# Optimization experiments

Hardware: AMD Instinct MI355X
Metric: run time of the kernel (lower is better)

Reference implementation:

```python
import jax, jax.numpy as jnp
import numpy as np

B, C, H, W = 4, 256, 64, 64
NUM_HEADS, HIDDEN = 2, 64


def setup_inputs() -> dict:
    key = jax.random.key(0)
    k1, k2, k3 = jax.random.split(key, 3)
    x = jax.random.normal(k1, (B, C, H, W), dtype=jnp.float32)
    # per-head fused QKV 1x1 conv weights: [num_heads, 3*hidden, C]
    embed_w = jax.random.normal(k2, (NUM_HEADS, 3 * HIDDEN, C), dtype=jnp.float32) * (2.0 / C) ** 0.5
    embed_b = jnp.zeros((NUM_HEADS, 3 * HIDDEN), dtype=jnp.float32)
    # output ConvTranspose2d kernel-1 weight: [in=hidden*heads, out=C]
    out_w = jax.random.normal(k3, (HIDDEN * NUM_HEADS, C), dtype=jnp.float32) * (2.0 / C) ** 0.5
    out_b = jnp.zeros((C,), dtype=jnp.float32)
    return {"x": x, "embed_w": embed_w, "embed_b": embed_b, "out_w": out_w, "out_b": out_b}


def reference(x, embed_w, embed_b, out_w, out_b):
    b, c, h, w = x.shape
    n = h * w
    scale = c ** (-0.5)  # scaled=True uses in_channels**-0.5
    xf = x.reshape(b, c, n)  # [B,C,N]
    # fused QKV projection for all heads (1x1 conv == channel matmul)
    qkv = jnp.einsum('bcn,hdc->bhdn', xf, embed_w) + embed_b[None, :, :, None]  # [B,Hh,3*hc,N]
    q, k, v = jnp.split(qkv, 3, axis=2)  # each [B,Hh,hc,N]
    # attention over flattened spatial positions
    attn = jax.nn.softmax(jnp.einsum('bhcm,bhcn->bhmn', q, k) * scale, axis=-1)  # [B,Hh,N,N]
    o = jnp.einsum('bhmn,bhcn->bhcm', attn, v)  # [B,Hh,hc,N]
    o = o.reshape(b, -1, n)  # concat heads -> [B, hc*Hh, N]
    # output 1x1 transpose conv: sum over input channel dim d of weight[d, c]
    out = jnp.einsum('bdn,dc->bcn', o, out_w) + out_b[None, :, None]
    out = out.reshape(b, c, h, w)
    return out + x  # residual=True
```

## Files before the change

kernel.cpp:

```cpp
#include <hip/hip_runtime.h>

#define B_SZ  4
#define C_IN  256
#define N_POS 4096
#define NH    2
#define HC    64

typedef __attribute__((ext_vector_type(8))) __bf16 bf16x8;
typedef __attribute__((ext_vector_type(4))) float  f32x4;
typedef unsigned short u16;

__device__ __forceinline__ u16 f2bf(float f) {
  unsigned u = __float_as_uint(f);
  u = u + 0x7FFF + ((u >> 16) & 1);
  return (u16)(u >> 16);
}

#if __has_builtin(__builtin_amdgcn_exp2f)
  #define EXP2(x) __builtin_amdgcn_exp2f(x)
#else
  #define EXP2(x) exp2f(x)
#endif

__device__ __forceinline__ unsigned cvtpk_bf16(float lo, float hi) {
  unsigned r;
  asm("v_cvt_pk_bf16_f32 %0, %1, %2" : "=v"(r) : "v"(lo), "v"(hi));
  return r;
}

__device__ __forceinline__ void gload_lds16(const void* g, void* l) {
  __builtin_amdgcn_global_load_lds(
      (const __attribute__((address_space(1))) unsigned*)g,
      (__attribute__((address_space(3))) unsigned*)l, 16, 0, 0);
}

__global__ __launch_bounds__(256) void k_prep_w(const float* __restrict__ ew,
                                                const float* __restrict__ ow,
                                                u16* __restrict__ wbf,
                                                u16* __restrict__ w2t) {
  int i = blockIdx.x * 256 + threadIdx.x;
  if (i < 384 * 256) wbf[i] = f2bf(ew[i]);
  if (i < 128 * 256) {
    int d = i >> 8, c = i & 255;
    w2t[c * 128 + d] = f2bf(ow[i]);
  }
}

__global__ __launch_bounds__(256) void k_qkv(const float* __restrict__ x,
                                             const u16* __restrict__ wbf,
                                             const float* __restrict__ eb,
                                             u16* __restrict__ Qt,
                                             u16* __restrict__ Kt,
                                             u16* __restrict__ Vs) {
  int id = blockIdx.x;
  int xcd = id & 7;
  int b = xcd >> 1, h = xcd & 1;
  int nt = id >> 3;
  int tid = threadIdx.x;
  int w = tid >> 6, l = tid & 63, lr = l & 15, lg = l >> 4;

  __shared__ __align__(16) u16 Xl[64 * 256];

  const float* xb = x + (size_t)b * C_IN * N_POS + nt*64;
  {
    int n = l;
#pragma unroll
    for (int pass = 0; pass < 8; pass++) {
      int oct = w + pass*4;
      int cb8 = oct * 8;
      float v[8];
#pragma unroll
      for (int j = 0; j < 8; j++) v[j] = xb[(size_t)(cb8 + j) * N_POS + n];
      union { bf16x8 vv; unsigned u[4]; } pk;
#pragma unroll
      for (int jj = 0; jj < 4; jj++) pk.u[jj] = cvtpk_bf16(v[2*jj], v[2*jj+1]);
      int slot = oct ^ ((n & 7) << 2);
      *(bf16x8*)&Xl[n * 256 + slot * 8] = pk.vv;
    }
  }
  __syncthreads();

  f32x4 acc[4][3] = {};
  const u16* brow[3];
#pragma unroll
  for (int i = 0; i < 3; i++)
    brow[i] = wbf + (size_t)(h*192 + (3*w + i)*16 + lr) * C_IN + lg*8;

#pragma unroll
  for (int kk = 0; kk < 8; kk++) {
    bf16x8 bfr[3];
#pragma unroll
    for (int i = 0; i < 3; i++) bfr[i] = *(const bf16x8*)(brow[i] + kk*32);
#pragma unroll
    for (int nsub = 0; nsub < 4; nsub++) {
      int n2 = nsub*16 + lr;
      int sp = (kk*4 + lg) ^ ((lr & 7) << 2);
      bf16x8 a = *(const bf16x8*)&Xl[n2*256 + sp*8];
#pragma unroll
      for (int i = 0; i < 3; i++)
        acc[nsub][i] = __builtin_amdgcn_mfma_f32_16x16x32_bf16(a, bfr[i], acc[nsub][i], 0, 0, 0);
    }
  }

  const float QSCALE = 0.0625f * 1.44269504088896f;
  int bh = b * NH + h;
#pragma unroll
  for (int i = 0; i < 3; i++) {
    int s3 = 3*w + i;
    int type = s3 >> 2, mf = s3 & 3;
    int cl = mf*16 + lr;
    float bias = eb[h*192 + type*64 + cl];
#pragma unroll
    for (int nsub = 0; nsub < 4; nsub++) {
      int n0 = nt*64 + nsub*16 + lg*4;
      if (type == 0) {
        u16* q = Qt + (size_t)bh * N_POS * HC;
#pragma unroll
        for (int r = 0; r < 4; r++) q[(size_t)(n0+r)*HC + cl] = f2bf((acc[nsub][i][r] + bias) * QSCALE);
      } else if (type == 1) {
        u16* kd = Kt + (size_t)bh * N_POS * HC;
#pragma unroll
        for (int r = 0; r < 4; r++) kd[(size_t)(n0+r)*HC + cl] = f2bf(acc[nsub][i][r] + bias);
      } else {
        u16* vd = Vs + (size_t)bh * (N_POS * HC);
        size_t idx = ((((size_t)nt*2 + (nsub>>1))*4 + lg)*64 + cl)*8 + 4*(nsub&1);
        ushort4 pk;
        pk.x = f2bf(acc[nsub][i][0] + bias);
        pk.y = f2bf(acc[nsub][i][1] + bias);
        pk.z = f2bf(acc[nsub][i][2] + bias);
        pk.w = f2bf(acc[nsub][i][3] + bias);
        *(ushort4*)(vd + idx) = pk;
      }
    }
  }
}

__device__ __forceinline__ void softmax_tile(f32x4 (&s)[4], f32x4& psv, float& rm,
                                             f32x4 (&o)[4]) {
  float mx = s[0][0];
#pragma unroll
  for (int nf = 0; nf < 4; nf++)
#pragma unroll
    for (int r = 0; r < 4; r++) mx = fmaxf(mx, s[nf][r]);
  mx = fmaxf(mx, __shfl_xor(mx, 16));
  mx = fmaxf(mx, __shfl_xor(mx, 32));
  float nm = fmaxf(rm, mx);
  float corr = EXP2(rm - nm);
  rm = nm;
#pragma unroll
  for (int r = 0; r < 4; r++) psv[r] *= corr;
#pragma unroll
  for (int nf = 0; nf < 4; nf++)
#pragma unroll
    for (int r = 0; r < 4; r++) {
      float p = EXP2(s[nf][r] - nm);
      s[nf][r] = p;
      psv[r] += p;
    }
#pragma unroll
  for (int cf = 0; cf < 4; cf++)
#pragma unroll
    for (int r = 0; r < 4; r++) o[cf][r] *= corr;
}

__global__ __launch_bounds__(1024, 4) void k_attn(const u16* __restrict__ Qt,
                                                  const u16* __restrict__ Kt,
                                                  const u16* __restrict__ Vs,
                                                  u16* __restrict__ Ot) {
  int id = blockIdx.x;
  int bh = id & 7;
  int mt = id >> 3;
  int b = bh >> 1, h = bh & 1;
  int tid = threadIdx.x;
  int wid = tid >> 6;
  int l = tid & 63, lr = l & 15, lg = l >> 4;
  int qi = wid & 3;
  int ci = wid >> 2;
  int m0 = mt*128 + qi*32;

  __shared__ __align__(16) char smem[131072];
  __shared__ float Lps[4][8][16];
  __shared__ float Lm[4][8][16];

  bf16x8 qf[2][2];
#pragma unroll
  for (int sub = 0; sub < 2; sub++) {
    const u16* qb = Qt + ((size_t)bh * N_POS + m0 + sub*16 + lr) * HC + lg*8;
    qf[sub][0] = *(const bf16x8*)qb;
    qf[sub][1] = *(const bf16x8*)(qb + 32);
  }

  const char* Kt_bh = (const char*)(Kt + (size_t)bh * N_POS * HC);
  const char* Vs_bh = (const char*)(Vs + (size_t)bh * N_POS * HC);
  int gtid = tid & 255;

  f32x4 o0[4] = {}, o1[4] = {};
  f32x4 ps0 = {}, ps1 = {};
  float rm0 = -1e30f, rm1 = -1e30f;
  int xr = (lr & 7) << 4;

  union PF { bf16x8 v; unsigned u[4]; };

  auto stage = [&](int tile, char* sb) {
    const char* ksrc = Kt_bh + (size_t)tile * 8192;
    const char* vsrc = Vs_bh + (size_t)tile * 8192;
#pragma unroll
    for (int j = 0; j < 2; j++) {
      int off = (j*256 + gtid) * 16;
      int koff = off ^ (((off >> 7) & 7) << 4);
      gload_lds16(ksrc + koff, sb + off);
      gload_lds16(vsrc + off, sb + 8192 + off);
    }
  };

  stage(ci*16, smem + ci*16384);
  __syncthreads();

  int buf = 0;
  for (int t = 0; t < 16; t++) {
    if (t < 15) stage(ci*16 + t + 1, smem + (buf^1)*65536 + ci*16384);

    const char* Kb = smem + buf*65536 + ci*16384;
    const char* Vb = Kb + 8192;

    f32x4 s0[4], s1[4];
    __builtin_amdgcn_s_setprio(1);
#pragma unroll
    for (int nf = 0; nf < 4; nf++) {
      const char* kr = Kb + (nf*16 + lr) * 128;
      bf16x8 k0 = *(const bf16x8*)(kr + ((lg*16)      ^ xr));
      bf16x8 k1 = *(const bf16x8*)(kr + ((lg*16 + 64) ^ xr));
      f32x4 z0 = {}, z1 = {};
      z0 = __builtin_amdgcn_mfma_f32_16x16x32_bf16(k0, qf[0][0], z0, 0, 0, 0);
      s0[nf] = __builtin_amdgcn_mfma_f32_16x16x32_bf16(k1, qf[0][1], z0, 0, 0, 0);
      z1 = __builtin_amdgcn_mfma_f32_16x16x32_bf16(k0, qf[1][0], z1, 0, 0, 0);
      s1[nf] = __builtin_amdgcn_mfma_f32_16x16x32_bf16(k1, qf[1][1], z1, 0, 0, 0);
    }
    __builtin_amdgcn_s_setprio(0);

    softmax_tile(s0, ps0, rm0, o0);
    softmax_tile(s1, ps1, rm1, o1);

    __builtin_amdgcn_s_setprio(1);
#pragma unroll
    for (int kk = 0; kk < 2; kk++) {
      PF pa, pb;
      pa.u[0] = cvtpk_bf16(s0[2*kk+0][0], s0[2*kk+0][1]);
      pa.u[1] = cvtpk_bf16(s0[2*kk+0][2], s0[2*kk+0][3]);
      pa.u[2] = cvtpk_bf16(s0[2*kk+1][0], s0[2*kk+1][1]);
      pa.u[3] = cvtpk_bf16(s0[2*kk+1][2], s0[2*kk+1][3]);
      pb.u[0] = cvtpk_bf16(s1[2*kk+0][0], s1[2*kk+0][1]);
      pb.u[1] = cvtpk_bf16(s1[2*kk+0][2], s1[2*kk+0][3]);
      pb.u[2] = cvtpk_bf16(s1[2*kk+1][0], s1[2*kk+1][1]);
      pb.u[3] = cvtpk_bf16(s1[2*kk+1][2], s1[2*kk+1][3]);
#pragma unroll
      for (int cf = 0; cf < 4; cf++) {
        bf16x8 vf = *(const bf16x8*)(Vb + (kk*4 + lg)*1024 + (cf*16 + lr)*16);
        o0[cf] = __builtin_amdgcn_mfma_f32_16x16x32_bf16(vf, pa.v, o0[cf], 0, 0, 0);
        o1[cf] = __builtin_amdgcn_mfma_f32_16x16x32_bf16(vf, pb.v, o1[cf], 0, 0, 0);
      }
    }
    __builtin_amdgcn_s_setprio(0);

    __syncthreads();
    buf ^= 1;
  }

  float psa = ps0[0] + ps0[1] + ps0[2] + ps0[3];
  psa += __shfl_xor(psa, 16);
  psa += __shfl_xor(psa, 32);
  float psb = ps1[0] + ps1[1] + ps1[2] + ps1[3];
  psb += __shfl_xor(psb, 16);
  psb += __shfl_xor(psb, 32);

  float (*Lo)[8][16][64] = (float (*)[8][16][64])smem;
#pragma unroll
  for (int cf = 0; cf < 4; cf++) {
    int colw = ((cf*16 + 4*lg) + 4*lr) & 63;
    *(f32x4*)&Lo[ci][qi*2+0][lr][colw] = o0[cf];
    *(f32x4*)&Lo[ci][qi*2+1][lr][colw] = o1[cf];
  }
  if (lg == 0) {
    Lps[ci][qi*2+0][lr] = psa; Lm[ci][qi*2+0][lr] = rm0;
    Lps[ci][qi*2+1][lr] = psb; Lm[ci][qi*2+1][lr] = rm1;
  }
  __syncthreads();

  int row = tid >> 3;
  int c0 = (tid & 7) * 8;
  int g = row >> 4, r2 = row & 15;
  float m0_ = Lm[0][g][r2], m1_ = Lm[1][g][r2];
  float m2_ = Lm[2][g][r2], m3_ = Lm[3][g][r2];
  float M = fmaxf(fmaxf(m0_, m1_), fmaxf(m2_, m3_));
  float w0 = EXP2(m0_ - M), w1 = EXP2(m1_ - M);
  float w2 = EXP2(m2_ - M), w3 = EXP2(m3_ - M);
  int ca = (c0 + 4*r2) & 63;
  int cb = (c0 + 4 + 4*r2) & 63;
  f32x4 accA, accB;
  {
    f32x4 a0 = *(const f32x4*)&Lo[0][g][r2][ca];
    f32x4 a1 = *(const f32x4*)&Lo[1][g][r2][ca];
    f32x4 a2 = *(const f32x4*)&Lo[2][g][r2][ca];
    f32x4 a3 = *(const f32x4*)&Lo[3][g][r2][ca];
#pragma unroll
    for (int i = 0; i < 4; i++) accA[i] = a0[i]*w0 + a1[i]*w1 + a2[i]*w2 + a3[i]*w3;
    f32x4 b0 = *(const f32x4*)&Lo[0][g][r2][cb];
    f32x4 b1 = *(const f32x4*)&Lo[1][g][r2][cb];
    f32x4 b2 = *(const f32x4*)&Lo[2][g][r2][cb];
    f32x4 b3 = *(const f32x4*)&Lo[3][g][r2][cb];
#pragma unroll
    for (int i = 0; i < 4; i++) accB[i] = b0[i]*w0 + b1[i]*w1 + b2[i]*w2 + b3[i]*w3;
  }
  float pst = Lps[0][g][r2]*w0 + Lps[1][g][r2]*w1
            + Lps[2][g][r2]*w2 + Lps[3][g][r2]*w3;
  float rinv = 1.0f / pst;
  u16* ob = Ot + ((size_t)b * N_POS + mt*128 + row) * (NH*HC) + h*HC + c0;
  uint4 st;
  st.x = cvtpk_bf16(accA[0]*rinv, accA[1]*rinv);
  st.y = cvtpk_bf16(accA[2]*rinv, accA[3]*rinv);
  st.z = cvtpk_bf16(accB[0]*rinv, accB[1]*rinv);
  st.w = cvtpk_bf16(accB[2]*rinv, accB[3]*rinv);
  *(uint4*)ob = st;
}

__global__ __launch_bounds__(256) void k_out(const u16* __restrict__ Ot,
                                             const u16* __restrict__ w2t,
                                             const float* __restrict__ obias,
                                             const float* __restrict__ x,
                                             float* __restrict__ out) {
  int b = blockIdx.z;
  int ct = blockIdx.y;
  int nt = blockIdx.x;
  int w = threadIdx.x >> 6, l = threadIdx.x & 63;
  int lr = l & 15, lg = l >> 4;

  const u16* arow = Ot + ((size_t)b * N_POS + nt*64 + w*16 + lr) * 128 + lg*8;
  const u16* brow = w2t + ((size_t)(ct*64) + lr) * 128 + lg*8;

  f32x4 acc[4] = {};
#pragma unroll
  for (int kk = 0; kk < 4; kk++) {
    bf16x8 a = *(const bf16x8*)(arow + kk*32);
#pragma unroll
    for (int cf = 0; cf < 4; cf++) {
      bf16x8 bf = *(const bf16x8*)(brow + (size_t)cf*16*128 + kk*32);
      acc[cf] = __builtin_amdgcn_mfma_f32_16x16x32_bf16(a, bf, acc[cf], 0, 0, 0);
    }
  }

  int n0 = nt*64 + w*16 + lg*4;
#pragma unroll
  for (int cf = 0; cf < 4; cf++) {
    int c = ct*64 + cf*16 + lr;
    float bias = obias[c];
    const float* xp = x + ((size_t)b * C_IN + c) * N_POS + n0;
    float* op = out + ((size_t)b * C_IN + c) * N_POS + n0;
    f32x4 xv = *(const f32x4*)xp;
    f32x4 rv;
#pragma unroll
    for (int i = 0; i < 4; i++) rv[i] = acc[cf][i] + bias + xv[i];
    *(f32x4*)op = rv;
  }
}

extern "C" void kernel_launch(void* const* d_in, const int* in_sizes, int n_in,
                              void* d_out, int out_size, void* d_ws, size_t ws_size,
                              hipStream_t stream) {
  const float* x  = (const float*)d_in[0];
  const float* ew = (const float*)d_in[1];
  const float* eb = (const float*)d_in[2];
  const float* ow = (const float*)d_in[3];
  const float* ob = (const float*)d_in[4];
  float* out = (float*)d_out;

  char* ws = (char*)d_ws;
  u16* wbf = (u16*)(ws + 0);
  u16* w2t = (u16*)(ws + 196608);
  u16* Qt  = (u16*)(ws + 262144);
  u16* Kt  = (u16*)(ws + 4456448);
  u16* Vs  = (u16*)(ws + 8650752);
  u16* Ot  = (u16*)(ws + 12845056);

  hipLaunchKernelGGL(k_prep_w, dim3(384), dim3(256), 0, stream, ew, ow, wbf, w2t);
  hipLaunchKernelGGL(k_qkv,  dim3(512),      dim3(256), 0, stream, x, wbf, eb, Qt, Kt, Vs);
  hipLaunchKernelGGL(k_attn, dim3(256),      dim3(1024), 0, stream, Qt, Kt, Vs, Ot);
  hipLaunchKernelGGL(k_out,  dim3(64, 4, 4), dim3(256), 0, stream, Ot, w2t, ob, x, out);
}
```

Before: 88.31 us.

## Halve attention block size, give each wave 64 query rows, defer softmax rescale

The attention kernel now runs 512 threads per block, with each wave owning four 16-row query sub-tiles instead of two. Each K and V fragment read from LDS therefore feeds twice as many MFMAs, cutting LDS traffic per FLOP, at the cost of more accumulator registers. Softmax also gains a lazy-rescale path: when no row max in the wave grows by more than 8 (log2 units) past the running max, the correction of O and the sum is skipped. The final combine loops over two passes to cover all 128 rows with fewer threads.

```diff
diff --git a/kernel.cpp b/kernel.cpp
--- a/kernel.cpp
+++ b/kernel.cpp
@@ -135,8 +135,10 @@
   }
 }
 
-__device__ __forceinline__ void softmax_tile(f32x4 (&s)[4], f32x4& psv, float& rm,
-                                             f32x4 (&o)[4]) {
+union PF { bf16x8 v; unsigned u[4]; };
+
+__device__ __forceinline__ void softmax_defer(f32x4 (&s)[4], f32x4& psv, float& rm,
+                                              f32x4 (&o)[4]) {
   float mx = s[0][0];
 #pragma unroll
   for (int nf = 0; nf < 4; nf++)
@@ -144,29 +146,40 @@
     for (int r = 0; r < 4; r++) mx = fmaxf(mx, s[nf][r]);
   mx = fmaxf(mx, __shfl_xor(mx, 16));
   mx = fmaxf(mx, __shfl_xor(mx, 32));
-  float nm = fmaxf(rm, mx);
-  float corr = EXP2(rm - nm);
-  rm = nm;
-#pragma unroll
-  for (int r = 0; r < 4; r++) psv[r] *= corr;
-#pragma unroll
-  for (int nf = 0; nf < 4; nf++)
-#pragma unroll
-    for (int r = 0; r < 4; r++) {
-      float p = EXP2(s[nf][r] - nm);
-      s[nf][r] = p;
-      psv[r] += p;
-    }
-#pragma unroll
-  for (int cf = 0; cf < 4; cf++)
-#pragma unroll
-    for (int r = 0; r < 4; r++) o[cf][r] *= corr;
-}
-
-__global__ __launch_bounds__(1024, 4) void k_attn(const u16* __restrict__ Qt,
-                                                  const u16* __restrict__ Kt,
-                                                  const u16* __restrict__ Vs,
-                                                  u16* __restrict__ Ot) {
+  if (__all(mx <= rm + 8.0f)) {
+#pragma unroll
+    for (int nf = 0; nf < 4; nf++)
+#pragma unroll
+      for (int r = 0; r < 4; r++) {
+        float p = EXP2(s[nf][r] - rm);
+        s[nf][r] = p;
+        psv[r] += p;
+      }
+  } else {
+    float nm = fmaxf(rm, mx);
+    float corr = EXP2(rm - nm);
+    rm = nm;
+#pragma unroll
+    for (int r = 0; r < 4; r++) psv[r] *= corr;
+#pragma unroll
+    for (int nf = 0; nf < 4; nf++)
+#pragma unroll
+      for (int r = 0; r < 4; r++) {
+        float p = EXP2(s[nf][r] - nm);
+        s[nf][r] = p;
+        psv[r] += p;
+      }
+#pragma unroll
+    for (int cf = 0; cf < 4; cf++)
+#pragma unroll
+      for (int r = 0; r < 4; r++) o[cf][r] *= corr;
+  }
+}
+
+__global__ __launch_bounds__(512, 2) void k_attn(const u16* __restrict__ Qt,
+                                                 const u16* __restrict__ Kt,
+                                                 const u16* __restrict__ Vs,
+                                                 u16* __restrict__ Ot) {
   int id = blockIdx.x;
   int bh = id & 7;
   int mt = id >> 3;
@@ -174,17 +187,17 @@
   int tid = threadIdx.x;
   int wid = tid >> 6;
   int l = tid & 63, lr = l & 15, lg = l >> 4;
-  int qi = wid & 3;
-  int ci = wid >> 2;
-  int m0 = mt*128 + qi*32;
+  int qi = wid & 1;
+  int ci = wid >> 1;
+  int m0 = mt*128 + qi*64;
 
   __shared__ __align__(16) char smem[131072];
   __shared__ float Lps[4][8][16];
   __shared__ float Lm[4][8][16];
 
-  bf16x8 qf[2][2];
-#pragma unroll
-  for (int sub = 0; sub < 2; sub++) {
+  bf16x8 qf[4][2];
+#pragma unroll
+  for (int sub = 0; sub < 4; sub++) {
     const u16* qb = Qt + ((size_t)bh * N_POS + m0 + sub*16 + lr) * HC + lg*8;
     qf[sub][0] = *(const bf16x8*)qb;
     qf[sub][1] = *(const bf16x8*)(qb + 32);
@@ -192,21 +205,21 @@
 
   const char* Kt_bh = (const char*)(Kt + (size_t)bh * N_POS * HC);
   const char* Vs_bh = (const char*)(Vs + (size_t)bh * N_POS * HC);
-  int gtid = tid & 255;
-
-  f32x4 o0[4] = {}, o1[4] = {};
-  f32x4 ps0 = {}, ps1 = {};
-  float rm0 = -1e30f, rm1 = -1e30f;
+  int gtid = tid & 127;
+
+  f32x4 o[4][4] = {};
+  f32x4 psv[4] = {};
+  float rm[4];
+#pragma unroll
+  for (int sub = 0; sub < 4; sub++) rm[sub] = -1e30f;
   int xr = (lr & 7) << 4;
-
-  union PF { bf16x8 v; unsigned u[4]; };
 
   auto stage = [&](int tile, char* sb) {
     const char* ksrc = Kt_bh + (size_t)tile * 8192;
     const char* vsrc = Vs_bh + (size_t)tile * 8192;
 #pragma unroll
-    for (int j = 0; j < 2; j++) {
-      int off = (j*256 + gtid) * 16;
+    for (int j = 0; j < 4; j++) {
+      int off = (j*128 + gtid) * 16;
       int koff = off ^ (((off >> 7) & 7) << 4);
       gload_lds16(ksrc + koff, sb + off);
       gload_lds16(vsrc + off, sb + 8192 + off);
@@ -223,104 +236,105 @@
     const char* Kb = smem + buf*65536 + ci*16384;
     const char* Vb = Kb + 8192;
 
-    f32x4 s0[4], s1[4];
+    f32x4 s[4][4];
     __builtin_amdgcn_s_setprio(1);
 #pragma unroll
     for (int nf = 0; nf < 4; nf++) {
       const char* kr = Kb + (nf*16 + lr) * 128;
       bf16x8 k0 = *(const bf16x8*)(kr + ((lg*16)      ^ xr));
       bf16x8 k1 = *(const bf16x8*)(kr + ((lg*16 + 64) ^ xr));
-      f32x4 z0 = {}, z1 = {};
-      z0 = __builtin_amdgcn_mfma_f32_16x16x32_bf16(k0, qf[0][0], z0, 0, 0, 0);
-      s0[nf] = __builtin_amdgcn_mfma_f32_16x16x32_bf16(k1, qf[0][1], z0, 0, 0, 0);
-      z1 = __builtin_amdgcn_mfma_f32_16x16x32_bf16(k0, qf[1][0], z1, 0, 0, 0);
-      s1[nf] = __builtin_amdgcn_mfma_f32_16x16x32_bf16(k1, qf[1][1], z1, 0, 0, 0);
+#pragma unroll
+      for (int sub = 0; sub < 4; sub++) {
+        f32x4 z = {};
+        z = __builtin_amdgcn_mfma_f32_16x16x32_bf16(k0, qf[sub][0], z, 0, 0, 0);
+        s[sub][nf] = __builtin_amdgcn_mfma_f32_16x16x32_bf16(k1, qf[sub][1], z, 0, 0, 0);
+      }
     }
     __builtin_amdgcn_s_setprio(0);
 
-    softmax_tile(s0, ps0, rm0, o0);
-    softmax_tile(s1, ps1, rm1, o1);
+    PF pf[4][2];
+#pragma unroll
+    for (int sub = 0; sub < 4; sub++) {
+      softmax_defer(s[sub], psv[sub], rm[sub], o[sub]);
+#pragma unroll
+      for (int kk = 0; kk < 2; kk++) {
+        pf[sub][kk].u[0] = cvtpk_bf16(s[sub][2*kk+0][0], s[sub][2*kk+0][1]);
+        pf[sub][kk].u[1] = cvtpk_bf16(s[sub][2*kk+0][2], s[sub][2*kk+0][3]);
+        pf[sub][kk].u[2] = cvtpk_bf16(s[sub][2*kk+1][0], s[sub][2*kk+1][1]);
+        pf[sub][kk].u[3] = cvtpk_bf16(s[sub][2*kk+1][2], s[sub][2*kk+1][3]);
+      }
+    }
 
     __builtin_amdgcn_s_setprio(1);
 #pragma unroll
-    for (int kk = 0; kk < 2; kk++) {
-      PF pa, pb;
-      pa.u[0] = cvtpk_bf16(s0[2*kk+0][0], s0[2*kk+0][1]);
-      pa.u[1] = cvtpk_bf16(s0[2*kk+0][2], s0[2*kk+0][3]);
-      pa.u[2] = cvtpk_bf16(s0[2*kk+1][0], s0[2*kk+1][1]);
-      pa.u[3] = cvtpk_bf16(s0[2*kk+1][2], s0[2*kk+1][3]);
-      pb.u[0] = cvtpk_bf16(s1[2*kk+0][0], s1[2*kk+0][1]);
-      pb.u[1] = cvtpk_bf16(s1[2*kk+0][2], s1[2*kk+0][3]);
-      pb.u[2] = cvtpk_bf16(s1[2*kk+1][0], s1[2*kk+1][1]);
-      pb.u[3] = cvtpk_bf16(s1[2*kk+1][2], s1[2*kk+1][3]);
+    for (int kk = 0; kk < 2; kk++)
 #pragma unroll
       for (int cf = 0; cf < 4; cf++) {
         bf16x8 vf = *(const bf16x8*)(Vb + (kk*4 + lg)*1024 + (cf*16 + lr)*16);
-        o0[cf] = __builtin_amdgcn_mfma_f32_16x16x32_bf16(vf, pa.v, o0[cf], 0, 0, 0);
-        o1[cf] = __builtin_amdgcn_mfma_f32_16x16x32_bf16(vf, pb.v, o1[cf], 0, 0, 0);
-      }
-    }
+#pragma unroll
+        for (int sub = 0; sub < 4; sub++)
+          o[sub][cf] = __builtin_amdgcn_mfma_f32_16x16x32_bf16(vf, pf[sub][kk].v, o[sub][cf], 0, 0, 0);
+      }
     __builtin_amdgcn_s_setprio(0);
 
     __syncthreads();
     buf ^= 1;
   }
 
-  float psa = ps0[0] + ps0[1] + ps0[2] + ps0[3];
-  psa += __shfl_xor(psa, 16);
-  psa += __shfl_xor(psa, 32);
-  float psb = ps1[0] + ps1[1] + ps1[2] + ps1[3];
-  psb += __shfl_xor(psb, 16);
-  psb += __shfl_xor(psb, 32);
-
   float (*Lo)[8][16][64] = (float (*)[8][16][64])smem;
 #pragma unroll
-  for (int cf = 0; cf < 4; cf++) {
-    int colw = ((cf*16 + 4*lg) + 4*lr) & 63;
-    *(f32x4*)&Lo[ci][qi*2+0][lr][colw] = o0[cf];
-    *(f32x4*)&Lo[ci][qi*2+1][lr][colw] = o1[cf];
-  }
-  if (lg == 0) {
-    Lps[ci][qi*2+0][lr] = psa; Lm[ci][qi*2+0][lr] = rm0;
-    Lps[ci][qi*2+1][lr] = psb; Lm[ci][qi*2+1][lr] = rm1;
+  for (int sub = 0; sub < 4; sub++) {
+    float ps = psv[sub][0] + psv[sub][1] + psv[sub][2] + psv[sub][3];
+    ps += __shfl_xor(ps, 16);
+    ps += __shfl_xor(ps, 32);
+    int qsub = qi*4 + sub;
+#pragma unroll
+    for (int cf = 0; cf < 4; cf++) {
+      int colw = ((cf*16 + 4*lg) + 4*lr) & 63;
+      *(f32x4*)&Lo[ci][qsub][lr][colw] = o[sub][cf];
+    }
+    if (lg == 0) { Lps[ci][qsub][lr] = ps; Lm[ci][qsub][lr] = rm[sub]; }
   }
   __syncthreads();
 
-  int row = tid >> 3;
-  int c0 = (tid & 7) * 8;
-  int g = row >> 4, r2 = row & 15;
-  float m0_ = Lm[0][g][r2], m1_ = Lm[1][g][r2];
-  float m2_ = Lm[2][g][r2], m3_ = Lm[3][g][r2];
-  float M = fmaxf(fmaxf(m0_, m1_), fmaxf(m2_, m3_));
-  float w0 = EXP2(m0_ - M), w1 = EXP2(m1_ - M);
-  float w2 = EXP2(m2_ - M), w3 = EXP2(m3_ - M);
-  int ca = (c0 + 4*r2) & 63;
-  int cb = (c0 + 4 + 4*r2) & 63;
-  f32x4 accA, accB;
-  {
-    f32x4 a0 = *(const f32x4*)&Lo[0][g][r2][ca];
-    f32x4 a1 = *(const f32x4*)&Lo[1][g][r2][ca];
-    f32x4 a2 = *(const f32x4*)&Lo[2][g][r2][ca];
-    f32x4 a3 = *(const f32x4*)&Lo[3][g][r2][ca];
-#pragma unroll
-    for (int i = 0; i < 4; i++) accA[i] = a0[i]*w0 + a1[i]*w1 + a2[i]*w2 + a3[i]*w3;
-    f32x4 b0 = *(const f32x4*)&Lo[0][g][r2][cb];
-    f32x4 b1 = *(const f32x4*)&Lo[1][g][r2][cb];
-    f32x4 b2 = *(const f32x4*)&Lo[2][g][r2][cb];
-    f32x4 b3 = *(const f32x4*)&Lo[3][g][r2][cb];
-#pragma unroll
-    for (int i = 0; i < 4; i++) accB[i] = b0[i]*w0 + b1[i]*w1 + b2[i]*w2 + b3[i]*w3;
-  }
-  float pst = Lps[0][g][r2]*w0 + Lps[1][g][r2]*w1
-            + Lps[2][g][r2]*w2 + Lps[3][g][r2]*w3;
-  float rinv = 1.0f / pst;
-  u16* ob = Ot + ((size_t)b * N_POS + mt*128 + row) * (NH*HC) + h*HC + c0;
-  uint4 st;
-  st.x = cvtpk_bf16(accA[0]*rinv, accA[1]*rinv);
-  st.y = cvtpk_bf16(accA[2]*rinv, accA[3]*rinv);
-  st.z = cvtpk_bf16(accB[0]*rinv, accB[1]*rinv);
-  st.w = cvtpk_bf16(accB[2]*rinv, accB[3]*rinv);
-  *(uint4*)ob = st;
+#pragma unroll
+  for (int pass = 0; pass < 2; pass++) {
+    int row = (tid >> 3) + pass*64;
+    int c0 = (tid & 7) * 8;
+    int g = row >> 4, r2 = row & 15;
+    float m0_ = Lm[0][g][r2], m1_ = Lm[1][g][r2];
+    float m2_ = Lm[2][g][r2], m3_ = Lm[3][g][r2];
+    float M = fmaxf(fmaxf(m0_, m1_), fmaxf(m2_, m3_));
+    float w0 = EXP2(m0_ - M), w1 = EXP2(m1_ - M);
+    float w2 = EXP2(m2_ - M), w3 = EXP2(m3_ - M);
+    int ca = (c0 + 4*r2) & 63;
+    int cb = (c0 + 4 + 4*r2) & 63;
+    f32x4 accA, accB;
+    {
+      f32x4 a0 = *(const f32x4*)&Lo[0][g][r2][ca];
+      f32x4 a1 = *(const f32x4*)&Lo[1][g][r2][ca];
+      f32x4 a2 = *(const f32x4*)&Lo[2][g][r2][ca];
+      f32x4 a3 = *(const f32x4*)&Lo[3][g][r2][ca];
+#pragma unroll
+      for (int i = 0; i < 4; i++) accA[i] = a0[i]*w0 + a1[i]*w1 + a2[i]*w2 + a3[i]*w3;
+      f32x4 b0 = *(const f32x4*)&Lo[0][g][r2][cb];
+      f32x4 b1 = *(const f32x4*)&Lo[1][g][r2][cb];
+      f32x4 b2 = *(const f32x4*)&Lo[2][g][r2][cb];
+      f32x4 b3 = *(const f32x4*)&Lo[3][g][r2][cb];
+#pragma unroll
+      for (int i = 0; i < 4; i++) accB[i] = b0[i]*w0 + b1[i]*w1 + b2[i]*w2 + b3[i]*w3;
+    }
+    float pst = Lps[0][g][r2]*w0 + Lps[1][g][r2]*w1
+              + Lps[2][g][r2]*w2 + Lps[3][g][r2]*w3;
+    float rinv = 1.0f / pst;
+    u16* ob = Ot + ((size_t)b * N_POS + mt*128 + row) * (NH*HC) + h*HC + c0;
+    uint4 st;
+    st.x = cvtpk_bf16(accA[0]*rinv, accA[1]*rinv);
+    st.y = cvtpk_bf16(accA[2]*rinv, accA[3]*rinv);
+    st.z = cvtpk_bf16(accB[0]*rinv, accB[1]*rinv);
+    st.w = cvtpk_bf16(accB[2]*rinv, accB[3]*rinv);
+    *(uint4*)ob = st;
+  }
 }
 
 __global__ __launch_bounds__(256) void k_out(const u16* __restrict__ Ot,
@@ -383,6 +397,6 @@
 
   hipLaunchKernelGGL(k_prep_w, dim3(384), dim3(256), 0, stream, ew, ow, wbf, w2t);
   hipLaunchKernelGGL(k_qkv,  dim3(512),      dim3(256), 0, stream, x, wbf, eb, Qt, Kt, Vs);
-  hipLaunchKernelGGL(k_attn, dim3(256),      dim3(1024), 0, stream, Qt, Kt, Vs, Ot);
+  hipLaunchKernelGGL(k_attn, dim3(256),      dim3(512), 0, stream, Qt, Kt, Vs, Ot);
   hipLaunchKernelGGL(k_out,  dim3(64, 4, 4), dim3(256), 0, stream, Ot, w2t, ob, x, out);
 }
```

Result: slower. 99.39 us (+12.5%).
